# Performance work log

Hardware: AMD Instinct MI355X
Metric: run time of the kernel (lower is better)

The kernel has to match this reference:

```python
import jax, jax.numpy as jnp
import numpy as np

NC = 6          # num_classes
RM = 16         # reg_max
TOPK = 10       # tal_topk
IMG = 640.0
STRIDES = (8, 16, 32)
BS = 32
NGT = 20        # GT boxes per image (uniform -> static max_boxes)


def _iou(b1, b2, ciou, eps=1e-7):
    x1 = jnp.maximum(b1[..., 0], b2[..., 0]); y1 = jnp.maximum(b1[..., 1], b2[..., 1])
    x2 = jnp.minimum(b1[..., 2], b2[..., 2]); y2 = jnp.minimum(b1[..., 3], b2[..., 3])
    inter = jnp.maximum(x2 - x1, 0.0) * jnp.maximum(y2 - y1, 0.0)
    w1 = jnp.maximum(b1[..., 2] - b1[..., 0], eps); h1 = jnp.maximum(b1[..., 3] - b1[..., 1], eps)
    w2 = jnp.maximum(b2[..., 2] - b2[..., 0], eps); h2 = jnp.maximum(b2[..., 3] - b2[..., 1], eps)
    union = w1 * h1 + w2 * h2 - inter + eps
    iou = inter / union
    if not ciou:
        return iou
    cw = jnp.maximum(b1[..., 2], b2[..., 2]) - jnp.minimum(b1[..., 0], b2[..., 0])
    ch = jnp.maximum(b1[..., 3], b2[..., 3]) - jnp.minimum(b1[..., 1], b2[..., 1])
    c2 = cw ** 2 + ch ** 2 + eps
    rho2 = ((b1[..., 0] + b1[..., 2] - b2[..., 0] - b2[..., 2]) ** 2
            + (b1[..., 1] + b1[..., 3] - b2[..., 1] - b2[..., 3]) ** 2) / 4.0
    v = (4.0 / (np.pi ** 2)) * (jnp.arctan(w2 / h2) - jnp.arctan(w1 / h1)) ** 2
    alpha = jax.lax.stop_gradient(v / (v - iou + (1.0 + eps)))
    return iou - (rho2 / c2 + v * alpha)


def _forward(p0, p1, p2, targets):
    bs = p0.shape[0]
    regs, clss, ancs, strs = [], [], [], []
    for p, s in zip((p0, p1, p2), STRIDES):
        b, c, h, w = p.shape
        p = jnp.transpose(p, (0, 2, 3, 1)).reshape(b, h * w, c)
        regs.append(p[..., :4 * RM].reshape(b, h * w, 4, RM))
        clss.append(p[..., 4 * RM:])
        gy, gx = jnp.meshgrid(jnp.arange(h), jnp.arange(w), indexing='ij')
        ancs.append(((jnp.stack([gx, gy], -1).astype(jnp.float32) + 0.5) * s).reshape(-1, 2))
        strs.append(jnp.full((h * w, 1), float(s), jnp.float32))
    pred_reg = jnp.concatenate(regs, 1)      # [bs, A, 4, RM]
    pred_cls = jnp.concatenate(clss, 1)      # [bs, A, NC]
    anchors = jnp.concatenate(ancs, 0)       # [A, 2] pixel coords
    stride_a = jnp.concatenate(strs, 0)      # [A, 1]
    A = anchors.shape[0]

    proj = jnp.arange(RM, dtype=jnp.float32)
    pd_dist = jnp.sum(jax.nn.softmax(pred_reg, -1) * proj, -1)       # [bs, A, 4]
    anc_b = jnp.broadcast_to(anchors[None], (bs, A, 2))
    pd_boxes = jnp.concatenate([anc_b - pd_dist[..., :2] * stride_a,
                                anc_b + pd_dist[..., 2:] * stride_a], -1)

    # GT parse: exactly NGT rows per image, grouped by image index (static reshape)
    G = targets.shape[0] // bs
    t = targets.reshape(bs, G, 6)
    gt_labels = t[..., 1]
    xywh = t[..., 2:6] * IMG
    gt_boxes = jnp.concatenate([xywh[..., :2] - xywh[..., 2:] / 2,
                                xywh[..., :2] + xywh[..., 2:] / 2], -1)  # [bs, G, 4]
    mask_gt = jnp.ones((bs, G, 1), jnp.float32)

    # ---- task-aligned assignment (on detached preds) ----
    pscore = jax.nn.sigmoid(jax.lax.stop_gradient(pred_cls))
    pbox_d = jax.lax.stop_gradient(pd_boxes)
    ious = _iou(gt_boxes[:, :, None, :], pbox_d[:, None, :, :], False)   # [bs, G, A]
    labels_i = gt_labels.astype(jnp.int32)
    scores = jnp.einsum('bac,bgc->bga', pscore, jax.nn.one_hot(labels_i, NC, dtype=pscore.dtype))
    align = (scores ** 0.5) * (ious ** 6.0)
    lt = anc_b[:, None, :, :] - gt_boxes[:, :, None, :2]
    rb = gt_boxes[:, :, None, 2:] - anc_b[:, None, :, :]
    in_gts = jnp.min(jnp.concatenate([lt, rb], -1), -1) > 1e-9
    align = align * in_gts * mask_gt
    _, tk_idx = jax.lax.top_k(align, TOPK)
    bi = jnp.arange(bs)[:, None, None]; gi = jnp.arange(G)[None, :, None]
    mask_pos = jnp.zeros((bs, G, A), bool).at[bi, gi, tk_idx].set(True)
    mask_pos = mask_pos & (align > 0)
    multi = jnp.sum(mask_pos, 1) > 1                                   # [bs, A]
    full = jnp.moveaxis(jax.nn.one_hot(jnp.argmax(align, 1), G), -1, 1) > 0.5
    mask_pos = jnp.where(multi[:, None, :], full, mask_pos)

    fg = jnp.any(mask_pos, 1)                                          # [bs, A]
    gt_idx = jnp.argmax(mask_pos, 1)                                   # [bs, A] (first True)
    tb = jnp.take_along_axis(gt_boxes, jnp.broadcast_to(gt_idx[..., None], (bs, A, 4)), axis=1)
    target_boxes = jnp.where(fg[..., None], tb, 0.0)
    t_lab = jnp.take_along_axis(labels_i, gt_idx, axis=1)
    iou_fg = jnp.maximum(jax.lax.stop_gradient(_iou(pd_boxes, target_boxes, False)), 0.0)
    norm_align = align / (jnp.max(align, -1, keepdims=True) + 1e-9)
    norm_g = jnp.take_along_axis(norm_align, gt_idx[:, None, :], axis=1)[:, 0, :]
    sval = jnp.where(fg, norm_g * iou_fg, 0.0)
    target_scores = sval[..., None] * jax.nn.one_hot(t_lab, NC, dtype=jnp.float32)

    # cls: BCE with logits, sum / num_anchors
    x = pred_cls
    bce = jnp.maximum(x, 0.0) - x * target_scores + jnp.log1p(jnp.exp(-jnp.abs(x)))
    loss_cls = jnp.sum(bce) / float(A)

    fgf = fg.astype(jnp.float32)
    num_pos = jnp.maximum(jnp.sum(fgf), 1.0)

    # bbox: 1 - CIoU over positives
    ciou = _iou(pd_boxes, target_boxes, True)
    loss_bbox = jnp.sum((1.0 - ciou) * fgf) / num_pos

    # DFL
    ltrb = jnp.concatenate([(anc_b - target_boxes[..., :2]) / stride_a,
                            (target_boxes[..., 2:] - anc_b) / stride_a], -1)
    ltrb = jnp.clip(ltrb, 0.0, RM - 1.01)
    tl = ltrb.astype(jnp.int32)
    wl = (tl + 1).astype(jnp.float32) - ltrb
    wr = ltrb - tl.astype(jnp.float32)
    logZ = jax.nn.logsumexp(pred_reg, -1)                              # [bs, A, 4]
    ce_l = logZ - jnp.take_along_axis(pred_reg, tl[..., None], -1)[..., 0]
    ce_r = logZ - jnp.take_along_axis(pred_reg, (tl + 1)[..., None], -1)[..., 0]
    loss_dfl = jnp.sum(jnp.sum(ce_l * wl + ce_r * wr, -1) * fgf) / num_pos

    l_cls = loss_cls * 1.0
    l_bbox = loss_bbox * 7.5
    l_dfl = loss_dfl * 1.5
    return jnp.stack([l_cls + l_bbox + l_dfl, l_cls, l_bbox, jnp.asarray(0.0, jnp.float32), l_dfl])


def setup_inputs() -> dict:
    key = jax.random.key(0)
    k0, k1, k2, k3, k4, k5 = jax.random.split(key, 6)
    C = 4 * RM + NC
    p0 = jax.random.normal(k0, (BS, C, 80, 80), jnp.float32)
    p1 = jax.random.normal(k1, (BS, C, 40, 40), jnp.float32)
    p2 = jax.random.normal(k2, (BS, C, 20, 20), jnp.float32)
    bidx = jnp.repeat(jnp.arange(BS), NGT).astype(jnp.float32)
    lab = jax.random.randint(k3, (BS * NGT,), 0, NC).astype(jnp.float32)
    cxcy = jax.random.uniform(k4, (BS * NGT, 2), minval=0.2, maxval=0.8)
    wh = jax.random.uniform(k5, (BS * NGT, 2), minval=0.05, maxval=0.3)
    targets = jnp.concatenate([bidx[:, None], lab[:, None], cxcy, wh], 1)
    return {"p0": p0, "p1": p1, "p2": p2, "targets": targets}


def reference(p0, p1, p2, targets):
    return _forward(p0, p1, p2, targets)
```

## Files before the change

### kernel.cpp

```cpp
#include <hip/hip_runtime.h>
#include <math.h>

#define NC 6
#define RM 16
#define TOPK 10
#define BSZ 32
#define G 20
#define A_TOT 8400
#define NBA (BSZ * A_TOT)
#define NBLK_PREP (NBA / 256)
#define NBLK_LOSS ((NBA + 255) / 256)
#define MAXCAND 1024

__device__ __forceinline__ void anchor_decode(int a, int& lvl, int& ai, int& w, int& hw, float& s) {
    if (a < 6400)      { lvl = 0; ai = a;        w = 80; hw = 6400; s = 8.f; }
    else if (a < 8000) { lvl = 1; ai = a - 6400; w = 40; hw = 1600; s = 16.f; }
    else               { lvl = 2; ai = a - 8000; w = 20; hw = 400;  s = 32.f; }
}

__device__ __forceinline__ float align_from(const float* __restrict__ trow, float logit,
                                            float4 box, float ax, float ay) {
    float cx = trow[2] * 640.f, cy = trow[3] * 640.f;
    float hwd = trow[4] * 320.f, hh = trow[5] * 320.f;
    float gx1 = cx - hwd, gy1 = cy - hh, gx2 = cx + hwd, gy2 = cy + hh;
    float mn = fminf(fminf(ax - gx1, ay - gy1), fminf(gx2 - ax, gy2 - ay));
    if (mn <= 1e-9f) return 0.f;
    const float eps = 1e-7f;
    float x1 = fmaxf(gx1, box.x), y1 = fmaxf(gy1, box.y);
    float x2 = fminf(gx2, box.z), y2 = fminf(gy2, box.w);
    float inter = fmaxf(x2 - x1, 0.f) * fmaxf(y2 - y1, 0.f);
    float gw = fmaxf(gx2 - gx1, eps), gh = fmaxf(gy2 - gy1, eps);
    float w2 = fmaxf(box.z - box.x, eps), h2 = fmaxf(box.w - box.y, eps);
    float uni = gw * gh + w2 * h2 - inter + eps;
    float iou = inter / uni;
    float sc = 1.f / (1.f + __expf(-logit));
    float i2 = iou * iou;
    return sqrtf(sc) * (i2 * i2 * i2);
}

__global__ __launch_bounds__(256) void k_prep(
        const float* __restrict__ p0, const float* __restrict__ p1, const float* __restrict__ p2,
        float* __restrict__ pd_boxes, float* __restrict__ logZ,
        unsigned int* __restrict__ mask, unsigned long long* __restrict__ packed,
        float* __restrict__ partial_prep) {
    int tid = blockIdx.x * 256 + threadIdx.x;
    int q = tid >> 2;
    int sd = tid & 3;
    int idx4 = q * 4;
    int b = idx4 / A_TOT, a4 = idx4 % A_TOT;
    int lvl, ai, w, hw; float s;
    anchor_decode(a4, lvl, ai, w, hw, s);
    const float* p = (lvl == 0) ? p0 : ((lvl == 1) ? p1 : p2);
    const float* base = p + (size_t)b * 70 * hw + ai;

    float4 se = make_float4(0, 0, 0, 0), sk = make_float4(0, 0, 0, 0);
    #pragma unroll
    for (int k = 0; k < RM; ++k) {
        float4 v = *(const float4*)(base + (size_t)(sd * RM + k) * hw);
        float fk = (float)k;
        float ex = __expf(v.x); se.x += ex; sk.x += ex * fk;
        float ey = __expf(v.y); se.y += ey; sk.y += ey * fk;
        float ez = __expf(v.z); se.z += ez; sk.z += ez * fk;
        float ew = __expf(v.w); se.w += ew; sk.w += ew * fk;
    }
    float d0 = sk.x / se.x, d1 = sk.y / se.y, d2 = sk.z / se.z, d3 = sk.w / se.w;
    float z0 = __logf(se.x), z1 = __logf(se.y), z2 = __logf(se.z), z3 = __logf(se.w);

    bool lo = (sd & 1) == 0, hi = (sd & 2) == 0;
    float ea0 = __shfl_xor(d0, 1), ea1 = __shfl_xor(d1, 1), ea2 = __shfl_xor(d2, 1), ea3 = __shfl_xor(d3, 1);
    float na0 = lo ? d0 : ea1, na1 = lo ? ea0 : d1, na2 = lo ? d2 : ea3, na3 = lo ? ea2 : d3;
    float fa0 = __shfl_xor(na0, 2), fa1 = __shfl_xor(na1, 2), fa2 = __shfl_xor(na2, 2), fa3 = __shfl_xor(na3, 2);
    float ma0 = hi ? na0 : fa2, ma1 = hi ? na1 : fa3, ma2 = hi ? fa0 : na2, ma3 = hi ? fa1 : na3;
    float za0 = __shfl_xor(z0, 1), za1 = __shfl_xor(z1, 1), za2 = __shfl_xor(z2, 1), za3 = __shfl_xor(z3, 1);
    float zb0 = lo ? z0 : za1, zb1 = lo ? za0 : z1, zb2 = lo ? z2 : za3, zb3 = lo ? za2 : z3;
    float zc0 = __shfl_xor(zb0, 2), zc1 = __shfl_xor(zb1, 2), zc2 = __shfl_xor(zb2, 2), zc3 = __shfl_xor(zb3, 2);
    float zd0 = hi ? zb0 : zc2, zd1 = hi ? zb1 : zc3, zd2 = hi ? zc0 : zb2, zd3 = hi ? zc1 : zb3;

    float ax = ((float)(ai % w + sd) + 0.5f) * s;
    float ay = ((float)(ai / w) + 0.5f) * s;
    ((float4*)pd_boxes)[tid] = make_float4(ax - ma0 * s, ay - ma1 * s, ax + ma2 * s, ay + ma3 * s);
    ((float4*)logZ)[tid] = make_float4(zd0, zd1, zd2, zd3);
    mask[tid] = 0u;
    packed[tid] = 0ull;

    float bce = 0.f;
    {
        float4 x = *(const float4*)(base + (size_t)(64 + sd) * hw);
        bce += fmaxf(x.x, 0.f) + __logf(1.f + __expf(-fabsf(x.x)));
        bce += fmaxf(x.y, 0.f) + __logf(1.f + __expf(-fabsf(x.y)));
        bce += fmaxf(x.z, 0.f) + __logf(1.f + __expf(-fabsf(x.z)));
        bce += fmaxf(x.w, 0.f) + __logf(1.f + __expf(-fabsf(x.w)));
        if (sd < 2) {
            float4 y = *(const float4*)(base + (size_t)(68 + sd) * hw);
            bce += fmaxf(y.x, 0.f) + __logf(1.f + __expf(-fabsf(y.x)));
            bce += fmaxf(y.y, 0.f) + __logf(1.f + __expf(-fabsf(y.y)));
            bce += fmaxf(y.z, 0.f) + __logf(1.f + __expf(-fabsf(y.z)));
            bce += fmaxf(y.w, 0.f) + __logf(1.f + __expf(-fabsf(y.w)));
        }
    }

    __shared__ float part[4];
    int lane = threadIdx.x & 63, wv = threadIdx.x >> 6;
    #pragma unroll
    for (int off = 32; off > 0; off >>= 1) bce += __shfl_down(bce, off);
    if (lane == 0) part[wv] = bce;
    __syncthreads();
    if (threadIdx.x == 0)
        partial_prep[blockIdx.x] = part[0] + part[1] + part[2] + part[3];
}

__device__ __forceinline__ bool cand_better(float av, int ai_, float bv, int bi_) {
    if (av > bv) return true;
    if (av < bv) return false;
    if (ai_ < 0) return false;
    if (bi_ < 0) return true;
    return ai_ < bi_;
}

__global__ __launch_bounds__(256) void k_align(
        const float* __restrict__ targets,
        const float* __restrict__ pd_boxes,
        const float* __restrict__ p0, const float* __restrict__ p1, const float* __restrict__ p2,
        float* __restrict__ amax, unsigned int* __restrict__ mask,
        unsigned long long* __restrict__ packed) {
    __shared__ float cval[MAXCAND];
    __shared__ int   cidx[MAXCAND];
    __shared__ int   cnt_s;
    __shared__ float wtv[4][TOPK];
    __shared__ int   wti[4][TOPK];
    __shared__ float redf[4];

    int bg = blockIdx.x;
    int b = bg / G;
    int g = bg % G;
    const float* t = targets + (size_t)bg * 6;
    int lab = (int)t[1];
    const float* cb[3];
    cb[0] = p0 + (size_t)b * 70 * 6400 + (size_t)(64 + lab) * 6400;
    cb[1] = p1 + (size_t)b * 70 * 1600 + (size_t)(64 + lab) * 1600;
    cb[2] = p2 + (size_t)b * 70 * 400  + (size_t)(64 + lab) * 400;
    const float4* pb = (const float4*)pd_boxes + (size_t)b * A_TOT;
    unsigned long long* pk_row = packed + (size_t)b * A_TOT;

    float cx = t[2] * 640.f, cy = t[3] * 640.f;
    float hwd = t[4] * 320.f, hh = t[5] * 320.f;
    float gx1 = cx - hwd, gy1 = cy - hh, gx2 = cx + hwd, gy2 = cy + hh;

    const float sv3[3] = {8.f, 16.f, 32.f};
    const int   wv3[3] = {80, 40, 20};
    const int   ov3[3] = {0, 6400, 8000};
    int x0[3], y0[3], nx[3], ncell[3];
    int ntot = 0;
    #pragma unroll
    for (int l = 0; l < 3; ++l) {
        float s = sv3[l]; int w = wv3[l];
        int xa = max(0, (int)floorf(gx1 / s - 0.5f));
        int xb = min(w - 1, (int)ceilf(gx2 / s - 0.5f));
        int ya = max(0, (int)floorf(gy1 / s - 0.5f));
        int yb = min(w - 1, (int)ceilf(gy2 / s - 0.5f));
        x0[l] = xa; y0[l] = ya;
        nx[l] = max(0, xb - xa + 1);
        int nyl = max(0, yb - ya + 1);
        ncell[l] = nx[l] * nyl;
        ntot += ncell[l];
    }

    if (threadIdx.x == 0) cnt_s = 0;
    __syncthreads();

    float lmax = -1.f;
    for (int i = threadIdx.x; i < ntot; i += 256) {
        int l = 0, loc = i;
        if (loc >= ncell[0]) { loc -= ncell[0]; l = 1; }
        if (l == 1 && loc >= ncell[1]) { loc -= ncell[1]; l = 2; }
        int iy = loc / nx[l], ix = loc % nx[l];
        ix += x0[l]; iy += y0[l];
        float s = sv3[l]; int w = wv3[l];
        float ax = ((float)ix + 0.5f) * s, ay = ((float)iy + 0.5f) * s;
        int a = ov3[l] + iy * w + ix;
        float logit = cb[l][iy * w + ix];
        float al = align_from(t, logit, pb[a], ax, ay);
        if (al > 0.f) {
            lmax = fmaxf(lmax, al);
            unsigned long long pkv =
                ((unsigned long long)__float_as_uint(al) << 32) | (0xFFFFFFFFu - (unsigned)g);
            atomicMax(&pk_row[a], pkv);
            int p = atomicAdd(&cnt_s, 1);
            if (p < MAXCAND) { cval[p] = al; cidx[p] = a; }
        }
    }
    int lane = threadIdx.x & 63, wv = threadIdx.x >> 6;
    #pragma unroll
    for (int off = 32; off > 0; off >>= 1) lmax = fmaxf(lmax, __shfl_xor(lmax, off));
    if (lane == 0) redf[wv] = lmax;
    __syncthreads();
    if (threadIdx.x == 0)
        amax[bg] = fmaxf(fmaxf(fmaxf(redf[0], redf[1]), fmaxf(redf[2], redf[3])), 0.f);

    int cnt = min(cnt_s, MAXCAND);
    float mv[MAXCAND / 256];
    int   mi[MAXCAND / 256];
    #pragma unroll
    for (int r = 0; r < MAXCAND / 256; ++r) {
        int p = threadIdx.x + r * 256;
        mv[r] = (p < cnt) ? cval[p] : -1.f;
        mi[r] = (p < cnt) ? cidx[p] : -1;
    }

    for (int it = 0; it < TOPK; ++it) {
        float v = -1.f; int vi = -1;
        #pragma unroll
        for (int r = 0; r < MAXCAND / 256; ++r)
            if (cand_better(mv[r], mi[r], v, vi)) { v = mv[r]; vi = mi[r]; }
        #pragma unroll
        for (int off = 1; off < 64; off <<= 1) {
            float ov = __shfl_xor(v, off);
            int   oi = __shfl_xor(vi, off);
            if (cand_better(ov, oi, v, vi)) { v = ov; vi = oi; }
        }
        if (vi < 0) {
            if (lane == 0)
                for (int j = it; j < TOPK; ++j) { wtv[wv][j] = -1.f; wti[wv][j] = -1; }
            break;
        }
        if (lane == 0) { wtv[wv][it] = v; wti[wv][it] = vi; }
        #pragma unroll
        for (int r = 0; r < MAXCAND / 256; ++r)
            if (mi[r] == vi) { mv[r] = -1.f; mi[r] = -1; }
    }
    __syncthreads();

    if (wv == 0) {
        float v4 = -1.f; int i4 = -1;
        if (lane < 4 * TOPK) { v4 = wtv[lane / TOPK][lane % TOPK]; i4 = wti[lane / TOPK][lane % TOPK]; }
        unsigned int* mrow = mask + (size_t)b * A_TOT;
        for (int it = 0; it < TOPK; ++it) {
            float v = v4; int vi = i4;
            #pragma unroll
            for (int off = 1; off < 64; off <<= 1) {
                float ov = __shfl_xor(v, off);
                int   oi = __shfl_xor(vi, off);
                if (cand_better(ov, oi, v, vi)) { v = ov; vi = oi; }
            }
            if (vi < 0) break;
            if (lane == 0) atomicOr(&mrow[vi], 1u << g);
            if (i4 == vi) { v4 = -1.f; i4 = -1; }
        }
    }
}

__global__ __launch_bounds__(256) void k_loss(
        const float* __restrict__ targets,
        const float* __restrict__ pd_boxes, const float* __restrict__ logZ,
        const float* __restrict__ amax, const unsigned int* __restrict__ mask,
        const unsigned long long* __restrict__ packed,
        const float* __restrict__ p0, const float* __restrict__ p1, const float* __restrict__ p2,
        float* __restrict__ partial) {
    int idx = blockIdx.x * 256 + threadIdx.x;
    float bce_s = 0.f, bbox_s = 0.f, dfl_s = 0.f, fg_s = 0.f;
    if (idx < NBA) {
        unsigned int m = mask[idx];
        if (m != 0u) {
            int b = idx / A_TOT, a = idx % A_TOT;
            int lvl, ai, w_, hw; float s;
            anchor_decode(a, lvl, ai, w_, hw, s);
            const float* p = (lvl == 0) ? p0 : ((lvl == 1) ? p1 : p2);
            const float* base = p + (size_t)b * 70 * hw + ai;
            float ax = ((ai % w_) + 0.5f) * s, ay = ((ai / w_) + 0.5f) * s;
            float4 box = ((const float4*)pd_boxes)[idx];
            int gidx; float al; bool have_al;
            if (__popc(m) > 1) {
                unsigned long long pk = packed[idx];
                gidx = (int)(0xFFFFFFFFu - (unsigned)(pk & 0xFFFFFFFFull));
                al = __uint_as_float((unsigned)(pk >> 32));
                have_al = true;
            } else {
                gidx = __ffs(m) - 1;
                al = 0.f;
                have_al = false;
            }
            const float* t = targets + ((size_t)b * G + gidx) * 6;
            int lab = (int)t[1];
            float logit = base[(size_t)(64 + lab) * hw];
            if (!have_al) al = align_from(t, logit, box, ax, ay);
            float cx = t[2] * 640.f, cy = t[3] * 640.f;
            float hwd = t[4] * 320.f, hh = t[5] * 320.f;
            float tbx1 = cx - hwd, tby1 = cy - hh, tbx2 = cx + hwd, tby2 = cy + hh;
            const float eps = 1e-7f;
            float x1 = fmaxf(box.x, tbx1), y1 = fmaxf(box.y, tby1);
            float x2 = fminf(box.z, tbx2), y2 = fminf(box.w, tby2);
            float inter = fmaxf(x2 - x1, 0.f) * fmaxf(y2 - y1, 0.f);
            float w1 = fmaxf(box.z - box.x, eps), h1 = fmaxf(box.w - box.y, eps);
            float w2 = fmaxf(tbx2 - tbx1, eps), h2 = fmaxf(tby2 - tby1, eps);
            float uni = w1 * h1 + w2 * h2 - inter + eps;
            float iou = inter / uni;
            float iou_fg = fmaxf(iou, 0.f);
            float sval = (al / (amax[b * G + gidx] + 1e-9f)) * iou_fg;
            bce_s = -logit * sval;
            fg_s = 1.f;
            float cw = fmaxf(box.z, tbx2) - fminf(box.x, tbx1);
            float ch = fmaxf(box.w, tby2) - fminf(box.y, tby1);
            float c2 = cw * cw + ch * ch + eps;
            float dx = box.x + box.z - tbx1 - tbx2;
            float dy = box.y + box.w - tby1 - tby2;
            float rho2 = (dx * dx + dy * dy) * 0.25f;
            float dv = atanf(w2 / h2) - atanf(w1 / h1);
            float v = 0.40528473f * dv * dv;
            float alpha = v / (v - iou + (1.f + eps));
            float ciou = iou - (rho2 / c2 + v * alpha);
            bbox_s = 1.f - ciou;
            float4 lzv = ((const float4*)logZ)[idx];
            float lz[4] = {lzv.x, lzv.y, lzv.z, lzv.w};
            float lt[4] = {(ax - tbx1) / s, (ay - tby1) / s, (tbx2 - ax) / s, (tby2 - ay) / s};
            #pragma unroll
            for (int sd = 0; sd < 4; ++sd) {
                float d = fminf(fmaxf(lt[sd], 0.f), (float)RM - 1.01f);
                int tl = (int)d;
                float wl = (float)(tl + 1) - d;
                float wr = d - (float)tl;
                float xl = base[(size_t)(sd * RM + tl) * hw];
                float xr = base[(size_t)(sd * RM + tl + 1) * hw];
                dfl_s += (lz[sd] - xl) * wl + (lz[sd] - xr) * wr;
            }
        }
    }
    __shared__ float part[4][4];
    int lane = threadIdx.x & 63, wv = threadIdx.x >> 6;
    #pragma unroll
    for (int off = 32; off > 0; off >>= 1) {
        bce_s  += __shfl_down(bce_s,  off);
        bbox_s += __shfl_down(bbox_s, off);
        dfl_s  += __shfl_down(dfl_s,  off);
        fg_s   += __shfl_down(fg_s,   off);
    }
    if (lane == 0) {
        part[wv][0] = bce_s; part[wv][1] = bbox_s;
        part[wv][2] = dfl_s; part[wv][3] = fg_s;
    }
    __syncthreads();
    if (threadIdx.x == 0) {
        float s0 = 0.f, s1 = 0.f, s2 = 0.f, s3 = 0.f;
        for (int i = 0; i < 4; ++i) {
            s0 += part[i][0]; s1 += part[i][1]; s2 += part[i][2]; s3 += part[i][3];
        }
        ((float4*)partial)[blockIdx.x] = make_float4(s0, s1, s2, s3);
    }
}

__global__ __launch_bounds__(256) void k_final(const float* __restrict__ partial,
                                               const float* __restrict__ partial_prep,
                                               float* __restrict__ out) {
    double s0 = 0., s1 = 0., s2 = 0., s3 = 0.;
    for (int i = threadIdx.x; i < NBLK_LOSS; i += 256) {
        float4 p = ((const float4*)partial)[i];
        s0 += p.x; s1 += p.y; s2 += p.z; s3 += p.w;
    }
    for (int i = threadIdx.x; i < NBLK_PREP; i += 256)
        s0 += partial_prep[i];
    #pragma unroll
    for (int off = 32; off > 0; off >>= 1) {
        s0 += __shfl_down(s0, off);
        s1 += __shfl_down(s1, off);
        s2 += __shfl_down(s2, off);
        s3 += __shfl_down(s3, off);
    }
    __shared__ double part[4][4];
    int lane = threadIdx.x & 63, wv = threadIdx.x >> 6;
    if (lane == 0) { part[wv][0] = s0; part[wv][1] = s1; part[wv][2] = s2; part[wv][3] = s3; }
    __syncthreads();
    if (threadIdx.x == 0) {
        double bce = 0., bbox = 0., dfl = 0., fgc = 0.;
        for (int i = 0; i < 4; ++i) {
            bce += part[i][0]; bbox += part[i][1]; dfl += part[i][2]; fgc += part[i][3];
        }
        double l_cls = bce / (double)A_TOT;
        double np_ = fmax(fgc, 1.0);
        double l_bbox = 7.5 * bbox / np_;
        double l_dfl = 1.5 * dfl / np_;
        out[0] = (float)(l_cls + l_bbox + l_dfl);
        out[1] = (float)l_cls;
        out[2] = (float)l_bbox;
        out[3] = 0.f;
        out[4] = (float)l_dfl;
    }
}

extern "C" void kernel_launch(void* const* d_in, const int* in_sizes, int n_in,
                              void* d_out, int out_size, void* d_ws, size_t ws_size,
                              hipStream_t stream) {
    const float* p0 = (const float*)d_in[0];
    const float* p1 = (const float*)d_in[1];
    const float* p2 = (const float*)d_in[2];
    const float* targets = (const float*)d_in[3];
    float* out = (float*)d_out;

    char* ws = (char*)d_ws;
    size_t off = 0;
    float* pd_boxes = (float*)(ws + off); off += (size_t)NBA * 4 * sizeof(float);
    float* logZ     = (float*)(ws + off); off += (size_t)NBA * 4 * sizeof(float);
    unsigned long long* packed = (unsigned long long*)(ws + off); off += (size_t)NBA * sizeof(unsigned long long);
    float* amax     = (float*)(ws + off); off += (size_t)BSZ * G * sizeof(float);
    unsigned int* mask = (unsigned int*)(ws + off); off += (size_t)NBA * sizeof(unsigned int);
    float* partial  = (float*)(ws + off); off += (size_t)NBLK_LOSS * 4 * sizeof(float);
    float* partial_prep = (float*)(ws + off); off += (size_t)NBLK_PREP * sizeof(float);

    k_prep<<<NBLK_PREP, 256, 0, stream>>>(p0, p1, p2, pd_boxes, logZ, mask, packed, partial_prep);
    k_align<<<BSZ * G, 256, 0, stream>>>(targets, pd_boxes, p0, p1, p2, amax, mask, packed);
    k_loss<<<NBLK_LOSS, 256, 0, stream>>>(targets, pd_boxes, logZ, amax, mask, packed,
                                          p0, p1, p2, partial);
    k_final<<<1, 256, 0, stream>>>(partial, partial_prep, out);
}
```

Baseline: 138.8 us.

## Fuse final reduction into loss kernel via last-block counters, process 4 anchors per thread

Removes the separate single-block final reduction launch by having the last-finishing loss block, detected through sharded atomic counters reset in the prep kernel, perform the global sum and write the outputs. Each loss thread now loads four mask words as a uint4 and loops over them, so the loss kernel uses a quarter as many blocks. This saves a kernel launch and cuts block count, at the cost of atomic traffic, threadfences, and more serial work per thread on sparse foreground anchors.

Measured after the change: 147.3 us. 6.2% more time.

```diff
diff --git a/kernel.cpp b/kernel.cpp
--- a/kernel.cpp
+++ b/kernel.cpp
@@ -9,7 +9,8 @@
 #define A_TOT 8400
 #define NBA (BSZ * A_TOT)
 #define NBLK_PREP (NBA / 256)
-#define NBLK_LOSS ((NBA + 255) / 256)
+#define NBLK_LOSS ((NBA + 1023) / 1024)
+#define NCNT 32
 #define MAXCAND 1024
 
 __device__ __forceinline__ void anchor_decode(int a, int& lvl, int& ai, int& w, int& hw, float& s) {
@@ -42,7 +43,7 @@
         const float* __restrict__ p0, const float* __restrict__ p1, const float* __restrict__ p2,
         float* __restrict__ pd_boxes, float* __restrict__ logZ,
         unsigned int* __restrict__ mask, unsigned long long* __restrict__ packed,
-        float* __restrict__ partial_prep) {
+        float* __restrict__ partial_prep, unsigned int* __restrict__ done) {
     int tid = blockIdx.x * 256 + threadIdx.x;
     int q = tid >> 2;
     int sd = tid & 3;
@@ -82,6 +83,7 @@
     ((float4*)logZ)[tid] = make_float4(zd0, zd1, zd2, zd3);
     mask[tid] = 0u;
     packed[tid] = 0ull;
+    if (blockIdx.x == 0 && threadIdx.x < NCNT + 1) done[threadIdx.x] = 0u;
 
     float bce = 0.f;
     {
@@ -255,17 +257,23 @@
         const float* __restrict__ amax, const unsigned int* __restrict__ mask,
         const unsigned long long* __restrict__ packed,
         const float* __restrict__ p0, const float* __restrict__ p1, const float* __restrict__ p2,
-        float* __restrict__ partial) {
-    int idx = blockIdx.x * 256 + threadIdx.x;
+        float* __restrict__ partial, const float* __restrict__ partial_prep,
+        unsigned int* __restrict__ done, float* __restrict__ out) {
+    int base = (blockIdx.x * 256 + threadIdx.x) * 4;
     float bce_s = 0.f, bbox_s = 0.f, dfl_s = 0.f, fg_s = 0.f;
-    if (idx < NBA) {
-        unsigned int m = mask[idx];
-        if (m != 0u) {
+    if (base < NBA) {
+        uint4 m4 = *(const uint4*)(mask + base);
+        unsigned int mm[4] = {m4.x, m4.y, m4.z, m4.w};
+        #pragma unroll 1
+        for (int j = 0; j < 4; ++j) {
+            unsigned int m = mm[j];
+            if (m == 0u) continue;
+            int idx = base + j;
             int b = idx / A_TOT, a = idx % A_TOT;
             int lvl, ai, w_, hw; float s;
             anchor_decode(a, lvl, ai, w_, hw, s);
             const float* p = (lvl == 0) ? p0 : ((lvl == 1) ? p1 : p2);
-            const float* base = p + (size_t)b * 70 * hw + ai;
+            const float* pbase = p + (size_t)b * 70 * hw + ai;
             float ax = ((ai % w_) + 0.5f) * s, ay = ((ai / w_) + 0.5f) * s;
             float4 box = ((const float4*)pd_boxes)[idx];
             int gidx; float al; bool have_al;
@@ -281,7 +289,7 @@
             }
             const float* t = targets + ((size_t)b * G + gidx) * 6;
             int lab = (int)t[1];
-            float logit = base[(size_t)(64 + lab) * hw];
+            float logit = pbase[(size_t)(64 + lab) * hw];
             if (!have_al) al = align_from(t, logit, box, ax, ay);
             float cx = t[2] * 640.f, cy = t[3] * 640.f;
             float hwd = t[4] * 320.f, hh = t[5] * 320.f;
@@ -296,8 +304,8 @@
             float iou = inter / uni;
             float iou_fg = fmaxf(iou, 0.f);
             float sval = (al / (amax[b * G + gidx] + 1e-9f)) * iou_fg;
-            bce_s = -logit * sval;
-            fg_s = 1.f;
+            bce_s += -logit * sval;
+            fg_s += 1.f;
             float cw = fmaxf(box.z, tbx2) - fminf(box.x, tbx1);
             float ch = fmaxf(box.w, tby2) - fminf(box.y, tby1);
             float c2 = cw * cw + ch * ch + eps;
@@ -308,7 +316,7 @@
             float v = 0.40528473f * dv * dv;
             float alpha = v / (v - iou + (1.f + eps));
             float ciou = iou - (rho2 / c2 + v * alpha);
-            bbox_s = 1.f - ciou;
+            bbox_s += 1.f - ciou;
             float4 lzv = ((const float4*)logZ)[idx];
             float lz[4] = {lzv.x, lzv.y, lzv.z, lzv.w};
             float lt[4] = {(ax - tbx1) / s, (ay - tby1) / s, (tbx2 - ax) / s, (tby2 - ay) / s};
@@ -318,8 +326,8 @@
                 int tl = (int)d;
                 float wl = (float)(tl + 1) - d;
                 float wr = d - (float)tl;
-                float xl = base[(size_t)(sd * RM + tl) * hw];
-                float xr = base[(size_t)(sd * RM + tl + 1) * hw];
+                float xl = pbase[(size_t)(sd * RM + tl) * hw];
+                float xr = pbase[(size_t)(sd * RM + tl + 1) * hw];
                 dfl_s += (lz[sd] - xl) * wl + (lz[sd] - xr) * wr;
             }
         }
@@ -338,40 +346,52 @@
         part[wv][2] = dfl_s; part[wv][3] = fg_s;
     }
     __syncthreads();
+
+    __shared__ int amlast;
     if (threadIdx.x == 0) {
         float s0 = 0.f, s1 = 0.f, s2 = 0.f, s3 = 0.f;
         for (int i = 0; i < 4; ++i) {
             s0 += part[i][0]; s1 += part[i][1]; s2 += part[i][2]; s3 += part[i][3];
         }
         ((float4*)partial)[blockIdx.x] = make_float4(s0, s1, s2, s3);
-    }
-}
-
-__global__ __launch_bounds__(256) void k_final(const float* __restrict__ partial,
-                                               const float* __restrict__ partial_prep,
-                                               float* __restrict__ out) {
-    double s0 = 0., s1 = 0., s2 = 0., s3 = 0.;
+        __threadfence();
+        int c = blockIdx.x & (NCNT - 1);
+        unsigned int quota = (c < (NBLK_LOSS & (NCNT - 1)))
+                           ? (unsigned)(NBLK_LOSS / NCNT + 1)
+                           : (unsigned)(NBLK_LOSS / NCNT);
+        int last = 0;
+        unsigned int old = atomicAdd(&done[c], 1u);
+        if (old == quota - 1u) {
+            unsigned int mo = atomicAdd(&done[NCNT], 1u);
+            if (mo == (unsigned)(NCNT - 1)) last = 1;
+        }
+        amlast = last;
+    }
+    __syncthreads();
+    if (!amlast) return;
+    __threadfence();
+
+    double a0 = 0., a1 = 0., a2 = 0., a3 = 0.;
     for (int i = threadIdx.x; i < NBLK_LOSS; i += 256) {
-        float4 p = ((const float4*)partial)[i];
-        s0 += p.x; s1 += p.y; s2 += p.z; s3 += p.w;
+        float4 pp = ((const float4*)partial)[i];
+        a0 += pp.x; a1 += pp.y; a2 += pp.z; a3 += pp.w;
     }
     for (int i = threadIdx.x; i < NBLK_PREP; i += 256)
-        s0 += partial_prep[i];
+        a0 += partial_prep[i];
     #pragma unroll
     for (int off = 32; off > 0; off >>= 1) {
-        s0 += __shfl_down(s0, off);
-        s1 += __shfl_down(s1, off);
-        s2 += __shfl_down(s2, off);
-        s3 += __shfl_down(s3, off);
-    }
-    __shared__ double part[4][4];
-    int lane = threadIdx.x & 63, wv = threadIdx.x >> 6;
-    if (lane == 0) { part[wv][0] = s0; part[wv][1] = s1; part[wv][2] = s2; part[wv][3] = s3; }
+        a0 += __shfl_down(a0, off);
+        a1 += __shfl_down(a1, off);
+        a2 += __shfl_down(a2, off);
+        a3 += __shfl_down(a3, off);
+    }
+    __shared__ double dpart[4][4];
+    if (lane == 0) { dpart[wv][0] = a0; dpart[wv][1] = a1; dpart[wv][2] = a2; dpart[wv][3] = a3; }
     __syncthreads();
     if (threadIdx.x == 0) {
         double bce = 0., bbox = 0., dfl = 0., fgc = 0.;
         for (int i = 0; i < 4; ++i) {
-            bce += part[i][0]; bbox += part[i][1]; dfl += part[i][2]; fgc += part[i][3];
+            bce += dpart[i][0]; bbox += dpart[i][1]; dfl += dpart[i][2]; fgc += dpart[i][3];
         }
         double l_cls = bce / (double)A_TOT;
         double np_ = fmax(fgc, 1.0);
@@ -403,10 +423,11 @@
     unsigned int* mask = (unsigned int*)(ws + off); off += (size_t)NBA * sizeof(unsigned int);
     float* partial  = (float*)(ws + off); off += (size_t)NBLK_LOSS * 4 * sizeof(float);
     float* partial_prep = (float*)(ws + off); off += (size_t)NBLK_PREP * sizeof(float);
-
-    k_prep<<<NBLK_PREP, 256, 0, stream>>>(p0, p1, p2, pd_boxes, logZ, mask, packed, partial_prep);
+    unsigned int* done = (unsigned int*)(ws + off); off += (size_t)(NCNT + 1) * sizeof(unsigned int);
+
+    k_prep<<<NBLK_PREP, 256, 0, stream>>>(p0, p1, p2, pd_boxes, logZ, mask, packed,
+                                          partial_prep, done);
     k_align<<<BSZ * G, 256, 0, stream>>>(targets, pd_boxes, p0, p1, p2, amax, mask, packed);
     k_loss<<<NBLK_LOSS, 256, 0, stream>>>(targets, pd_boxes, logZ, amax, mask, packed,
-                                          p0, p1, p2, partial);
-    k_final<<<1, 256, 0, stream>>>(partial, partial_prep, out);
-}
+                                          p0, p1, p2, partial, partial_prep, done, out);
+}
```
